# Performance work log

Hardware: AMD Instinct MI355X
Metric: run time of the kernel (lower is better)

## Reference

```python
import jax, jax.numpy as jnp
import numpy as np

B, N, D_IN, D_OUT = 4, 2048, 1024, 1024

def setup_inputs() -> dict:
    key = jax.random.key(0)
    ks = jax.random.split(key, 7)
    s_in = 1.0 / np.sqrt(D_IN)
    return {
        "X": jax.random.normal(ks[0], (B, N, D_IN), dtype=jnp.float32),
        "Wq": jax.random.uniform(ks[1], (D_IN, D_OUT), jnp.float32, -s_in, s_in),
        "bq": jax.random.uniform(ks[2], (D_OUT,), jnp.float32, -s_in, s_in),
        "Wk": jax.random.uniform(ks[3], (D_IN, D_OUT), jnp.float32, -s_in, s_in),
        "bk": jax.random.uniform(ks[4], (D_OUT,), jnp.float32, -s_in, s_in),
        "Wv": jax.random.uniform(ks[5], (D_IN, D_OUT), jnp.float32, -s_in, s_in),
        "bv": jax.random.uniform(ks[6], (D_OUT,), jnp.float32, -s_in, s_in),
    }

def reference(X, Wq, bq, Wk, bk, Wv, bv):
    # QKV projections: [B,N,D_in] @ [D_in,D_out] -> [B,N,D_out]
    q = jnp.einsum('bnd,de->bne', X, Wq) + bq
    k = jnp.einsum('bnd,de->bne', X, Wk) + bk
    v = jnp.einsum('bnd,de->bne', X, Wv) + bv
    # Unscaled attention (faithful: original has no 1/sqrt(d))
    scores = jnp.einsum('bne,bme->bnm', q, k)  # [B,N,N]
    weights = jax.nn.softmax(scores, axis=-1)
    return jnp.einsum('bnm,bme->bne', weights, v)
```

## Files before the change

### kernel.cpp

```cpp
#include <hip/hip_runtime.h>
#include <hip/hip_bf16.h>
#include <hip/hip_fp16.h>
#include <stdint.h>
#include <math.h>


typedef unsigned short ushort_t;
typedef __attribute__((ext_vector_type(8))) _Float16  f16x8;
typedef __attribute__((ext_vector_type(4))) _Float16  f16x4;
typedef __attribute__((ext_vector_type(4))) float     f32x4;

__device__ __forceinline__ void async_load16(const void* g, void* l) {
  __builtin_amdgcn_global_load_lds(
      (const __attribute__((address_space(1))) void*)g,
      (__attribute__((address_space(3))) void*)l, 16, 0, 0);
}

#define BARR do { __builtin_amdgcn_sched_barrier(0); \
                  __builtin_amdgcn_s_barrier();      \
                  __builtin_amdgcn_s_barrier();      \
                  __builtin_amdgcn_sched_barrier(0); } while (0)
#undef BARR
#define BARR do { __builtin_amdgcn_sched_barrier(0); \
                  __builtin_amdgcn_s_barrier();      \
                  __builtin_amdgcn_sched_barrier(0); } while (0)

#define A0OFF 0
#define B0OFF 16384
#define A1OFF 32768
#define B1OFF 49152

template<int SHIFT>
__device__ __forceinline__ void stage_half(const ushort_t* __restrict__ gb,
                                           int k0, int q, ushort_t* lt, int t)
{
#pragma unroll
  for (int j = 0; j < 2; ++j) {
    const int i   = j * 64 + (t >> 3);
    const int row = ((i >> SHIFT) << (SHIFT + 1)) | (q << SHIFT) | (i & ((1 << SHIFT) - 1));
    const int ch  = (t & 7) ^ (row & 7);
    async_load16(gb + (long)row * 1024 + k0 + ch * 8, lt + row * 64 + (t & 7) * 8);
  }
}

#define RD_A(TP, QM)                                                          \
  do { _Pragma("unroll") for (int m_ = 0; m_ < 4; ++m_) {                     \
    af[m_][0] = *(const f16x8*)&(TP)[(arow0 + (QM)*64 + m_*16) * 64 + ck0];   \
    af[m_][1] = *(const f16x8*)&(TP)[(arow0 + (QM)*64 + m_*16) * 64 + ck1];   \
  } } while (0)

#define RD_B(TP, QN)                                                          \
  do { _Pragma("unroll") for (int n_ = 0; n_ < 2; ++n_) {                     \
    bf[n_][0] = *(const f16x8*)&(TP)[(brow0 + (QN)*32 + n_*16) * 64 + ck0];   \
    bf[n_][1] = *(const f16x8*)&(TP)[(brow0 + (QN)*32 + n_*16) * 64 + ck1];   \
  } } while (0)

#define MM(QM, QN)                                                            \
  do { __builtin_amdgcn_s_setprio(1);                                         \
  _Pragma("unroll") for (int kh_ = 0; kh_ < 2; ++kh_)                         \
    _Pragma("unroll") for (int m_ = 0; m_ < 4; ++m_)                          \
      _Pragma("unroll") for (int n_ = 0; n_ < 2; ++n_)                        \
        acc[(QM)*4+m_][(QN)*2+n_] = __builtin_amdgcn_mfma_f32_16x16x32_f16(   \
            af[m_][kh_], bf[n_][kh_], acc[(QM)*4+m_][(QN)*2+n_], 0, 0, 0);    \
  __builtin_amdgcn_s_setprio(0); } while (0)

template<bool LAST>
__device__ __forceinline__ void iter256(const ushort_t* __restrict__ Ab,
                                        const ushort_t* __restrict__ Bb,
                                        ushort_t* lds, f32x4 (&acc)[8][4],
                                        int ka, int t, int arow0, int brow0,
                                        int ck0, int ck1)
{
  const int kb = ka + 64, kc = ka + 128, kd = ka + 192;
  f16x8 af[4][2], bf[2][2];

  RD_A(lds + A0OFF, 0); RD_B(lds + B0OFF, 0);
  stage_half<5>(Bb, kb, 0, lds + B1OFF, t);
  BARR; MM(0, 0); BARR;

  RD_B(lds + B0OFF, 1);
  if constexpr (!LAST) stage_half<6>(Ab, kc, 0, lds + A0OFF, t);
  BARR; MM(0, 1); BARR;

  RD_A(lds + A0OFF, 1);
  if constexpr (!LAST) stage_half<5>(Bb, kc, 1, lds + B0OFF, t);
  BARR; MM(1, 1); BARR;

  RD_B(lds + B0OFF, 0);
  if constexpr (!LAST) stage_half<6>(Ab, kc, 1, lds + A0OFF, t);
  BARR; MM(1, 0);
  if constexpr (LAST) asm volatile("s_waitcnt vmcnt(0)" ::: "memory");
  else                asm volatile("s_waitcnt vmcnt(6)" ::: "memory");
  BARR;

  RD_A(lds + A1OFF, 0); RD_B(lds + B1OFF, 0);
  if constexpr (!LAST) stage_half<5>(Bb, kc, 0, lds + B0OFF, t);
  BARR; MM(0, 0); BARR;

  RD_B(lds + B1OFF, 1);
  if constexpr (!LAST) stage_half<6>(Ab, kd, 0, lds + A1OFF, t);
  BARR; MM(0, 1); BARR;

  RD_A(lds + A1OFF, 1);
  if constexpr (!LAST) stage_half<5>(Bb, kd, 1, lds + B1OFF, t);
  BARR; MM(1, 1); BARR;

  RD_B(lds + B1OFF, 0);
  if constexpr (!LAST) stage_half<6>(Ab, kd, 1, lds + A1OFF, t);
  BARR; MM(1, 0);
  if constexpr (!LAST) asm volatile("s_waitcnt vmcnt(6)" ::: "memory");
  BARR;
}

__device__ __forceinline__ void gemm256(const ushort_t* __restrict__ Ab,
                                        const ushort_t* __restrict__ Bb,
                                        ushort_t* lds, f32x4 (&acc)[8][4])
{
  const int t    = threadIdx.x;
  const int lane = t & 63;
  const int wave = t >> 6;
  const int wr   = wave >> 2;
  const int wc   = wave & 3;
  const int arow0 = wr * 128 + (lane & 15);
  const int brow0 = wc * 64  + (lane & 15);
  const int ck0 = (((lane >> 4)    ) ^ (lane & 7)) * 8;
  const int ck1 = ((4 + (lane >> 4)) ^ (lane & 7)) * 8;

  stage_half<6>(Ab,  0, 0, lds + A0OFF, t);
  stage_half<5>(Bb,  0, 1, lds + B0OFF, t);
  stage_half<6>(Ab,  0, 1, lds + A0OFF, t);
  stage_half<5>(Bb,  0, 0, lds + B0OFF, t);
  stage_half<6>(Ab, 64, 0, lds + A1OFF, t);
  stage_half<5>(Bb, 64, 1, lds + B1OFF, t);
  stage_half<6>(Ab, 64, 1, lds + A1OFF, t);
  asm volatile("s_waitcnt vmcnt(6)" ::: "memory");
  BARR;

#pragma unroll 1
  for (int it = 0; it < 7; ++it)
    iter256<false>(Ab, Bb, lds, acc, it * 128, t, arow0, brow0, ck0, ck1);
  iter256<true>(Ab, Bb, lds, acc, 896, t, arow0, brow0, ck0, ck1);
}

#define NA0 0
#define NB0 16384
#define NA1 24576
#define NB1 40960

__device__ __forceinline__ void stage_h256(const ushort_t* __restrict__ gb, long ldk,
                                           int k0, int q, ushort_t* lt, int t)
{
#pragma unroll
  for (int j = 0; j < 2; ++j) {
    const int i   = j * 64 + (t >> 3);
    const int row = ((i >> 5) << 6) | (q << 5) | (i & 31);
    const int ch  = (t & 7) ^ (row & 7);
    async_load16(gb + (long)row * ldk + k0 + ch * 8, lt + row * 64 + (t & 7) * 8);
  }
}

__device__ __forceinline__ void stage_h128(const ushort_t* __restrict__ gb, long ldk,
                                           int k0, int q, ushort_t* lt, int t)
{
  const int i   = t >> 3;
  const int row = ((i >> 5) << 6) | (q << 5) | (i & 31);
  const int ch  = (t & 7) ^ (row & 7);
  async_load16(gb + (long)row * ldk + k0 + ch * 8, lt + row * 64 + (t & 7) * 8);
}

#define RD_A4(SET, BASE, QM)                                                  \
  do { _Pragma("unroll") for (int m_ = 0; m_ < 2; ++m_) {                     \
    SET[m_][0] = *(const f16x8*)&lds[(BASE) + (arow_l + (QM)*32 + m_*16) * 64 + ck0]; \
    SET[m_][1] = *(const f16x8*)&lds[(BASE) + (arow_l + (QM)*32 + m_*16) * 64 + ck1]; \
  } } while (0)

#define RD_B4(SET, BASE)                                                      \
  do { _Pragma("unroll") for (int q_ = 0; q_ < 2; ++q_)                       \
    _Pragma("unroll") for (int n_ = 0; n_ < 2; ++n_) {                        \
      SET[q_][n_][0] = *(const f16x8*)&lds[(BASE) + (brow_l + q_*32 + n_*16) * 64 + ck0]; \
      SET[q_][n_][1] = *(const f16x8*)&lds[(BASE) + (brow_l + q_*32 + n_*16) * 64 + ck1]; \
    } } while (0)

#define MM16(AS, BS, QM)                                                      \
  do { __builtin_amdgcn_s_setprio(1);                                         \
  _Pragma("unroll") for (int kh_ = 0; kh_ < 2; ++kh_)                         \
    _Pragma("unroll") for (int m_ = 0; m_ < 2; ++m_)                          \
      _Pragma("unroll") for (int n_ = 0; n_ < 2; ++n_) {                      \
        acc[(QM)*2+m_][n_]   = __builtin_amdgcn_mfma_f32_16x16x32_f16(        \
            AS[m_][kh_], BS[0][n_][kh_], acc[(QM)*2+m_][n_], 0, 0, 0);        \
        acc[(QM)*2+m_][2+n_] = __builtin_amdgcn_mfma_f32_16x16x32_f16(        \
            AS[m_][kh_], BS[1][n_][kh_], acc[(QM)*2+m_][2+n_], 0, 0, 0);      \
      }                                                                       \
  __builtin_amdgcn_s_setprio(0); } while (0)

#define MM16S(AS, BS, QM, SC)                                                 \
  do { __builtin_amdgcn_s_setprio(1);                                         \
  _Pragma("unroll") for (int m_ = 0; m_ < 2; ++m_)                            \
    _Pragma("unroll") for (int kh_ = 0; kh_ < 2; ++kh_) {                     \
      const f16x8 as_ = AS[m_][kh_] * (_Float16)(SC)[(QM)*2+m_];              \
      _Pragma("unroll") for (int n_ = 0; n_ < 2; ++n_) {                      \
        acc[(QM)*2+m_][n_]   = __builtin_amdgcn_mfma_f32_16x16x32_f16(        \
            as_, BS[0][n_][kh_], acc[(QM)*2+m_][n_], 0, 0, 0);                \
        acc[(QM)*2+m_][2+n_] = __builtin_amdgcn_mfma_f32_16x16x32_f16(        \
            as_, BS[1][n_][kh_], acc[(QM)*2+m_][2+n_], 0, 0, 0);              \
      } }                                                                     \
  __builtin_amdgcn_s_setprio(0); } while (0)

template<bool LAST>
__device__ __forceinline__ void iterRA(const ushort_t* __restrict__ Ab,
                                       const ushort_t* __restrict__ Bb,
                                       long lda, long ldb,
                                       ushort_t* lds, f32x4 (&acc)[4][4],
                                       int ka, int t, int arow_l, int brow_l,
                                       int ck0, int ck1,
                                       f16x8 (&aF)[2][2], f16x8 (&aG)[2][2],
                                       f16x8 (&bF)[2][2][2], f16x8 (&bG)[2][2][2])
{
  const int kc = ka + 128, kd = ka + 192;

  RD_A4(aG, NA0, 1);
  if constexpr (!LAST) { stage_h256(Ab, lda, kc, 0, lds + NA0, t);
                         stage_h128(Bb, ldb, kc, 0, lds + NB0, t); }
  BARR;
  MM16(aF, bF, 0);
  if constexpr (LAST) asm volatile("s_waitcnt vmcnt(0)" ::: "memory");
  else                asm volatile("s_waitcnt vmcnt(3)" ::: "memory");
  BARR;

  RD_A4(aF, NA1, 0);
  RD_B4(bG, NB1);
  if constexpr (!LAST) { stage_h256(Ab, lda, kc, 1, lds + NA0, t);
                         stage_h128(Bb, ldb, kc, 1, lds + NB0, t); }
  BARR;
  MM16(aG, bF, 1);
  BARR;

  RD_A4(aG, NA1, 1);
  if constexpr (!LAST) { stage_h256(Ab, lda, kd, 0, lds + NA1, t);
                         stage_h128(Bb, ldb, kd, 0, lds + NB1, t); }
  BARR;
  MM16(aF, bG, 0);
  if constexpr (!LAST) asm volatile("s_waitcnt vmcnt(3)" ::: "memory");
  BARR;

  if constexpr (!LAST) {
    RD_A4(aF, NA0, 0);
    RD_B4(bF, NB0);
    stage_h256(Ab, lda, kd, 1, lds + NA1, t);
    stage_h128(Bb, ldb, kd, 1, lds + NB1, t);
  }
  BARR;
  MM16(aG, bG, 1);
  BARR;
}

template<bool LAST>
__device__ __forceinline__ void pv_iterRA(const ushort_t* __restrict__ Ab,
                                          const ushort_t* __restrict__ Bb,
                                          ushort_t* lds, const float (*ScL)[256],
                                          f32x4 (&acc)[4][4],
                                          int ka, int t, int arow_l, int brow_l,
                                          int ck0, int ck1,
                                          f16x8 (&aF)[2][2], f16x8 (&aG)[2][2],
                                          f16x8 (&bF)[2][2][2], f16x8 (&bG)[2][2][2])
{
  const int kc = ka + 128, kd = ka + 192;
  const int cba = ka >> 6;
  float sa4[4], sb4[4];
#pragma unroll
  for (int s = 0; s < 4; ++s) {
    sa4[s] = ScL[cba][arow_l + s * 16];
    sb4[s] = ScL[cba + 1][arow_l + s * 16];
  }

  RD_A4(aG, NA0, 1);
  if constexpr (!LAST) { stage_h256(Ab, 2048, kc, 0, lds + NA0, t);
                         stage_h128(Bb, 2048, kc, 0, lds + NB0, t); }
  BARR;
  MM16S(aF, bF, 0, sa4);
  if constexpr (LAST) asm volatile("s_waitcnt vmcnt(0)" ::: "memory");
  else                asm volatile("s_waitcnt vmcnt(3)" ::: "memory");
  BARR;

  RD_A4(aF, NA1, 0);
  RD_B4(bG, NB1);
  if constexpr (!LAST) { stage_h256(Ab, 2048, kc, 1, lds + NA0, t);
                         stage_h128(Bb, 2048, kc, 1, lds + NB0, t); }
  BARR;
  MM16S(aG, bF, 1, sa4);
  BARR;

  RD_A4(aG, NA1, 1);
  if constexpr (!LAST) { stage_h256(Ab, 2048, kd, 0, lds + NA1, t);
                         stage_h128(Bb, 2048, kd, 0, lds + NB1, t); }
  BARR;
  MM16S(aF, bG, 0, sb4);
  if constexpr (!LAST) asm volatile("s_waitcnt vmcnt(3)" ::: "memory");
  BARR;

  if constexpr (!LAST) {
    RD_A4(aF, NA0, 0);
    RD_B4(bF, NB0);
    stage_h256(Ab, 2048, kd, 1, lds + NA1, t);
    stage_h128(Bb, 2048, kd, 1, lds + NB1, t);
  }
  BARR;
  MM16S(aG, bG, 1, sb4);
  BARR;
}

#define PROLOGUE_RA(LDA, LDB)                               \
  do {                                                      \
    stage_h256(Ab, (LDA),  0, 0, lds + NA0, t);             \
    stage_h128(Bb, (LDB),  0, 0, lds + NB0, t);             \
    stage_h256(Ab, (LDA),  0, 1, lds + NA0, t);             \
    stage_h128(Bb, (LDB),  0, 1, lds + NB0, t);             \
    asm volatile("s_waitcnt vmcnt(0)" ::: "memory");        \
    BARR;                                                   \
    RD_A4(aF, NA0, 0);                                      \
    RD_B4(bF, NB0);                                         \
    stage_h256(Ab, (LDA), 64, 0, lds + NA1, t);             \
    stage_h128(Bb, (LDB), 64, 0, lds + NB1, t);             \
    stage_h256(Ab, (LDA), 64, 1, lds + NA1, t);             \
    stage_h128(Bb, (LDB), 64, 1, lds + NB1, t);             \
    BARR;                                                   \
  } while (0)

__global__ __launch_bounds__(512, 2)
void qkproj_kernel(const ushort_t* __restrict__ A, const ushort_t* __restrict__ BT,
                   const float* __restrict__ bq, const float* __restrict__ bk,
                   __half* __restrict__ Qh, __half* __restrict__ Kh)
{
  __shared__ __align__(16) ushort_t lds[65536];

  const int nb = gridDim.x * gridDim.y;
  int id = blockIdx.y * gridDim.x + blockIdx.x;
  id = (id & 7) * (nb >> 3) + (id >> 3);
  const int bx = id % gridDim.x;
  const int by = id / gridDim.x;

  const ushort_t* Ab = A  + (long)by * 256 * 1024;
  const ushort_t* Bb = BT + (long)bx * 256 * 1024;

  f32x4 acc[8][4];
  const f32x4 zero = {0.0f, 0.0f, 0.0f, 0.0f};
#pragma unroll
  for (int i = 0; i < 8; ++i)
#pragma unroll
    for (int j = 0; j < 4; ++j) acc[i][j] = zero;

  gemm256(Ab, Bb, lds, acc);

  const int t = threadIdx.x, lane = t & 63, wave = t >> 6;
  const int wr = wave >> 2, wc = wave & 3;
  const int er = (lane >> 4) * 4, ec = lane & 15;
  const int tgt = bx >> 2;
  const float* bias = (tgt == 0) ? bq : bk;
  __half* o = (tgt == 0) ? Qh : Kh;

#pragma unroll
  for (int ni = 0; ni < 4; ++ni) {
    const int col = (bx & 3) * 256 + wc * 64 + ni * 16 + ec;
    const float bval = bias[col];
#pragma unroll
    for (int mi = 0; mi < 8; ++mi) {
      const long grow0 = (long)by * 256 + wr * 128 + mi * 16 + er;
#pragma unroll
      for (int r = 0; r < 4; ++r)
        o[(grow0 + r) * 1024 + col] = __float2half(acc[mi][ni][r] + bval);
    }
  }
}

__global__ __launch_bounds__(512, 2)
void vproj_kernel(const ushort_t* __restrict__ A, const ushort_t* __restrict__ BT,
                  const float* __restrict__ bvp, ushort_t* __restrict__ Vt)
{
  __shared__ __align__(16) ushort_t lds[49152];

  const int nb = gridDim.x * gridDim.y;
  int id = blockIdx.y * gridDim.x + blockIdx.x;
  id = (id & 7) * (nb >> 3) + (id >> 3);
  const int bx = id % gridDim.x;
  const int by = id / gridDim.x;

  const ushort_t* Ab = A  + (long)by * 256 * 1024;
  const ushort_t* Bb = BT + (long)(16 + bx) * 128 * 1024;

  const int t    = threadIdx.x;
  const int lane = t & 63;
  const int wave = t >> 6;
  const int wr   = wave >> 1;
  const int wc   = wave & 1;
  const int arow_l = wr * 64 + (lane & 15);
  const int brow_l = wc * 64 + (lane & 15);
  const int ck0 = (((lane >> 4)    ) ^ (lane & 7)) * 8;
  const int ck1 = ((4 + (lane >> 4)) ^ (lane & 7)) * 8;

  f32x4 acc[4][4];
  const f32x4 zero = {0.0f, 0.0f, 0.0f, 0.0f};
#pragma unroll
  for (int i = 0; i < 4; ++i)
#pragma unroll
    for (int j = 0; j < 4; ++j) acc[i][j] = zero;

  f16x8 aF[2][2], aG[2][2], bF[2][2][2], bG[2][2][2];

  PROLOGUE_RA(1024, 1024);
#pragma unroll 1
  for (int it = 0; it < 7; ++it)
    iterRA<false>(Ab, Bb, 1024, 1024, lds, acc, it * 128, t, arow_l, brow_l,
                  ck0, ck1, aF, aG, bF, bG);
  iterRA<true>(Ab, Bb, 1024, 1024, lds, acc, 896, t, arow_l, brow_l,
               ck0, ck1, aF, aG, bF, bG);

  const int er = (lane >> 4) * 4, ec = lane & 15;
#pragma unroll
  for (int ni = 0; ni < 4; ++ni) {
    const int col = bx * 128 + wc * 64 + ni * 16 + ec;
    const float bval = bvp[col];
#pragma unroll
    for (int mi = 0; mi < 4; ++mi) {
      const long grow0 = (long)by * 256 + wr * 64 + mi * 16 + er;
      const long b  = grow0 >> 11;
      const long ml = grow0 & 2047;
      f16x4 v4;
#pragma unroll
      for (int r = 0; r < 4; ++r) v4[r] = (_Float16)(acc[mi][ni][r] + bval);
      *(f16x4*)&Vt[b * 2097152 + (long)col * 2048 + ml] = v4;
    }
  }
}

__global__ __launch_bounds__(512, 2)
void qkattn_kernel(const ushort_t* __restrict__ Q, const ushort_t* __restrict__ Kh,
                   __half* __restrict__ S, float* __restrict__ PM, float* __restrict__ PS)
{
  __shared__ __align__(16) ushort_t lds[65536];

  const int nb = gridDim.x * gridDim.y;
  int id = blockIdx.y * gridDim.x + blockIdx.x;
  id = (id & 7) * (nb >> 3) + (id >> 3);
  const int bx = id % gridDim.x;
  const int by = id / gridDim.x;
  const long z = blockIdx.z;

  const ushort_t* Ab = Q  + z * 2048 * 1024 + (long)by * 256 * 1024;
  const ushort_t* Bb = Kh + z * 2048 * 1024 + (long)bx * 256 * 1024;
  __half* Sb = S + z * 2048 * 2048;

  f32x4 acc[8][4];
  const f32x4 zero = {0.0f, 0.0f, 0.0f, 0.0f};
#pragma unroll
  for (int i = 0; i < 8; ++i)
#pragma unroll
    for (int j = 0; j < 4; ++j) acc[i][j] = zero;

  gemm256(Ab, Bb, lds, acc);

  const int t = threadIdx.x, lane = t & 63, wave = t >> 6;
  const int wr = wave >> 2, wc = wave & 3;
  const int er = (lane >> 4) * 4, ec = lane & 15;
  const int cc = bx * 4 + wc;
  float* PMb = PM + z * 32 * 2048 + (long)cc * 2048;
  float* PSb = PS + z * 32 * 2048 + (long)cc * 2048;

#pragma unroll
  for (int m8 = 0; m8 < 8; ++m8)
#pragma unroll
    for (int r = 0; r < 4; ++r) {
      float m = fmaxf(fmaxf(acc[m8][0][r], acc[m8][1][r]),
                      fmaxf(acc[m8][2][r], acc[m8][3][r]));
      m = fmaxf(m, __shfl_xor(m, 1));
      m = fmaxf(m, __shfl_xor(m, 2));
      m = fmaxf(m, __shfl_xor(m, 4));
      m = fmaxf(m, __shfl_xor(m, 8));
      float s = 0.0f;
#pragma unroll
      for (int n4 = 0; n4 < 4; ++n4) {
        const float e = __expf(acc[m8][n4][r] - m);
        acc[m8][n4][r] = e;
        s += e;
      }
      s += __shfl_xor(s, 1);
      s += __shfl_xor(s, 2);
      s += __shfl_xor(s, 4);
      s += __shfl_xor(s, 8);
      if (ec == 0) {
        const long row = (long)by * 256 + wr * 128 + m8 * 16 + er + r;
        PMb[row] = m;
        PSb[row] = s;
      }
    }

#pragma unroll
  for (int n4 = 0; n4 < 4; ++n4) {
    const long col = (long)bx * 256 + wc * 64 + n4 * 16 + ec;
#pragma unroll
    for (int m8 = 0; m8 < 8; ++m8)
#pragma unroll
      for (int r = 0; r < 4; ++r) {
        const long grow = (long)by * 256 + wr * 128 + m8 * 16 + er + r;
        Sb[grow * 2048 + col] = __float2half(acc[m8][n4][r]);
      }
  }
}

__global__ __launch_bounds__(512, 2)
void pv_ra_kernel(const ushort_t* __restrict__ S, const ushort_t* __restrict__ Vt,
                  const float* __restrict__ PM, const float* __restrict__ PS,
                  float* __restrict__ Out)
{
  __shared__ __align__(16) ushort_t lds[49152];
  __shared__ float ScL[32][256];

  const int nb = gridDim.x * gridDim.y;
  int id = blockIdx.y * gridDim.x + blockIdx.x;
  id = (id & 7) * (nb >> 3) + (id >> 3);
  const int bx = id % gridDim.x;
  const int by = id / gridDim.x;
  const long z = blockIdx.z;

  const ushort_t* Ab = S  + z * 4194304 + (long)by * 256 * 2048;
  const ushort_t* Bb = Vt + z * 2097152 + (long)bx * 128 * 2048;
  float* Cb = Out + z * 2048 * 1024;

  const int t = threadIdx.x;

  if (t < 256) {
    const long row = (long)by * 256 + t;
    const float* PMb = PM + z * 32 * 2048;
    const float* PSb = PS + z * 32 * 2048;
    float pm[32];
    float m = -3.4e38f;
#pragma unroll
    for (int cb = 0; cb < 32; ++cb) {
      pm[cb] = PMb[(long)cb * 2048 + row];
      m = fmaxf(m, pm[cb]);
    }
    float l = 0.0f;
#pragma unroll
    for (int cb = 0; cb < 32; ++cb)
      l += PSb[(long)cb * 2048 + row] * __expf(pm[cb] - m);
    const float inv = 1.0f / l;
#pragma unroll
    for (int cb = 0; cb < 32; ++cb)
      ScL[cb][t] = __expf(pm[cb] - m) * inv;
  }
  __syncthreads();

  const int lane = t & 63;
  const int wave = t >> 6;
  const int wr   = wave >> 1;
  const int wc   = wave & 1;
  const int arow_l = wr * 64 + (lane & 15);
  const int brow_l = wc * 64 + (lane & 15);
  const int ck0 = (((lane >> 4)    ) ^ (lane & 7)) * 8;
  const int ck1 = ((4 + (lane >> 4)) ^ (lane & 7)) * 8;

  f32x4 acc[4][4];
  const f32x4 zero = {0.0f, 0.0f, 0.0f, 0.0f};
#pragma unroll
  for (int i = 0; i < 4; ++i)
#pragma unroll
    for (int j = 0; j < 4; ++j) acc[i][j] = zero;

  f16x8 aF[2][2], aG[2][2], bF[2][2][2], bG[2][2][2];

  PROLOGUE_RA(2048, 2048);
#pragma unroll 1
  for (int it = 0; it < 15; ++it)
    pv_iterRA<false>(Ab, Bb, lds, ScL, acc, it * 128, t, arow_l, brow_l,
                     ck0, ck1, aF, aG, bF, bG);
  pv_iterRA<true>(Ab, Bb, lds, ScL, acc, 1920, t, arow_l, brow_l,
                  ck0, ck1, aF, aG, bF, bG);

  const int er = (lane >> 4) * 4, ec = lane & 15;
#pragma unroll
  for (int ni = 0; ni < 4; ++ni) {
    const int gcol = bx * 128 + wc * 64 + ni * 16 + ec;
#pragma unroll
    for (int mi = 0; mi < 4; ++mi) {
#pragma unroll
      for (int r = 0; r < 4; ++r) {
        const long grow = (long)by * 256 + wr * 64 + mi * 16 + er + r;
        Cb[grow * 1024 + gcol] = acc[mi][ni][r];
      }
    }
  }
}

__global__ __launch_bounds__(256)
void prep_kernel(const float* __restrict__ W0, const float* __restrict__ W1,
                 const float* __restrict__ W2, __half* __restrict__ dstW,
                 const float* __restrict__ X, __half* __restrict__ Xh)
{
  __shared__ float tile[32][33];
  const int z = blockIdx.z;
  if (z < 3) {
    const float* src = (z == 0) ? W0 : (z == 1) ? W1 : W2;
    __half* d = dstW + (long)z * 1024 * 1024;
    const int c0 = blockIdx.x * 32;
    const int r0 = blockIdx.y * 32;
    const int tx = threadIdx.x & 31;
    const int ty = threadIdx.x >> 5;
#pragma unroll
    for (int i = 0; i < 32; i += 8)
      tile[ty + i][tx] = src[(long)(r0 + ty + i) * 1024 + (c0 + tx)];
    __syncthreads();
#pragma unroll
    for (int i = 0; i < 32; i += 8)
      d[(long)(c0 + ty + i) * 1024 + (r0 + tx)] = __float2half(tile[tx][ty + i]);
  } else {
    const int bid = blockIdx.y * gridDim.x + blockIdx.x;
    const long i = (((long)(z - 3) * 1024 + bid) * 256 + threadIdx.x) * 8;
    const float4 a = *(const float4*)(X + i);
    const float4 b = *(const float4*)(X + i + 4);
    f16x8 h;
    h[0] = (_Float16)a.x; h[1] = (_Float16)a.y; h[2] = (_Float16)a.z; h[3] = (_Float16)a.w;
    h[4] = (_Float16)b.x; h[5] = (_Float16)b.y; h[6] = (_Float16)b.z; h[7] = (_Float16)b.w;
    *(f16x8*)((ushort_t*)Xh + i) = h;
  }
}

extern "C" void kernel_launch(void* const* d_in, const int* in_sizes, int n_in,
                              void* d_out, int out_size, void* d_ws, size_t ws_size,
                              hipStream_t stream)
{
  const int  Bb = 4, Nn = 2048, Dd = 1024;
  const long BN = (long)Bb * Nn;

  const float* X  = (const float*)d_in[0];
  const float* Wq = (const float*)d_in[1];
  const float* bq = (const float*)d_in[2];
  const float* Wk = (const float*)d_in[3];
  const float* bk = (const float*)d_in[4];
  const float* Wv = (const float*)d_in[5];
  const float* bv = (const float*)d_in[6];
  float* Out      = (float*)d_out;

  uint8_t* w = (uint8_t*)d_ws;
  ushort_t* Wt = (ushort_t*)w;  w += (size_t)3 * Dd * Dd * 2;

  const size_t statsBytes = (size_t)Bb * 32 * Nn * 4;
  const size_t fullNeed = (size_t)3 * Dd * Dd * 2
                        + 4 * ((size_t)BN * Dd * 2)
                        + (size_t)Bb * Nn * Nn * 2
                        + 2 * statsBytes;

  if (ws_size >= fullNeed) {
    ushort_t* Xh = (ushort_t*)w;  w += (size_t)BN * Dd * 2;
    ushort_t* Q  = (ushort_t*)w;  w += (size_t)BN * Dd * 2;
    ushort_t* Kb = (ushort_t*)w;  w += (size_t)BN * Dd * 2;
    ushort_t* Vt = (ushort_t*)w;  w += (size_t)BN * Dd * 2;
    ushort_t* S  = (ushort_t*)w;  w += (size_t)Bb * Nn * Nn * 2;
    float*    PM = (float*)w;     w += statsBytes;
    float*    PS = (float*)w;

    prep_kernel<<<dim3(32, 32, 7), 256, 0, stream>>>(Wq, Wk, Wv, (__half*)Wt, X, (__half*)Xh);

    qkproj_kernel<<<dim3(8, BN / 256, 1), 512, 0, stream>>>(
        Xh, Wt, bq, bk, (__half*)Q, (__half*)Kb);

    vproj_kernel<<<dim3(8, BN / 256, 1), 512, 0, stream>>>(Xh, Wt, bv, Vt);

    qkattn_kernel<<<dim3(Nn / 256, Nn / 256, Bb), 512, 0, stream>>>(
        Q, Kb, (__half*)S, PM, PS);

    pv_ra_kernel<<<dim3(Dd / 128, Nn / 256, Bb), 512, 0, stream>>>(
        S, Vt, PM, PS, Out);
  } else {
    ushort_t* Xh = (ushort_t*)w;  w += (size_t)Nn * Dd * 2;
    ushort_t* Q  = (ushort_t*)w;  w += (size_t)Nn * Dd * 2;
    ushort_t* Kb = (ushort_t*)w;  w += (size_t)Nn * Dd * 2;
    ushort_t* Vt = (ushort_t*)w;  w += (size_t)Nn * Dd * 2;
    ushort_t* S  = (ushort_t*)w;  w += (size_t)Nn * Nn * 2;
    float*    PM = (float*)w;     w += (size_t)32 * Nn * 4;
    float*    PS = (float*)w;

    for (int b = 0; b < Bb; ++b) {
      const float* Xb = X + (long)b * Nn * Dd;
      prep_kernel<<<dim3(32, 32, b == 0 ? 4 : 1), 256, 0, stream>>>(
          Wq, Wk, Wv, (__half*)Wt, Xb, (__half*)Xh);
      qkproj_kernel<<<dim3(8, Nn / 256, 1), 512, 0, stream>>>(
          Xh, Wt, bq, bk, (__half*)Q, (__half*)Kb);
      vproj_kernel<<<dim3(8, Nn / 256, 1), 512, 0, stream>>>(Xh, Wt, bv, Vt);
      qkattn_kernel<<<dim3(Nn / 256, Nn / 256, 1), 512, 0, stream>>>(
          Q, Kb, (__half*)S, PM, PS);
      pv_ra_kernel<<<dim3(Dd / 128, Nn / 256, 1), 512, 0, stream>>>(
          S, Vt, PM, PS, Out + (long)b * Nn * Dd);
    }
  }
}
```

Measured before the change: 258.7 us.

## Stage GEMM epilogues through LDS for coalesced 16-byte global stores

The qkproj, vproj and qkattn epilogues now write fp16 results into a per-wave LDS tile, then read them back as 8-element vectors so each global store is a coalesced 16-byte write instead of scattered 2-byte stores. The qkattn softmax row statistics are batched so that all max and sum shuffle reductions run over 32 rows at once, which gives more instruction-level parallelism. The vproj launch is moved ahead of qkproj, and a duplicated BARR definition is cleaned up. The LDS staging adds extra LDS traffic and waitcnt stalls, and it relies on the mainloop LDS buffers being free when the epilogue reuses them.

```diff
diff --git a/kernel.cpp b/kernel.cpp
--- a/kernel.cpp
+++ b/kernel.cpp
@@ -18,12 +18,10 @@
 
 #define BARR do { __builtin_amdgcn_sched_barrier(0); \
                   __builtin_amdgcn_s_barrier();      \
-                  __builtin_amdgcn_s_barrier();      \
                   __builtin_amdgcn_sched_barrier(0); } while (0)
-#undef BARR
-#define BARR do { __builtin_amdgcn_sched_barrier(0); \
-                  __builtin_amdgcn_s_barrier();      \
-                  __builtin_amdgcn_sched_barrier(0); } while (0)
+
+#define LGKM0 do { asm volatile("s_waitcnt lgkmcnt(0)" ::: "memory"); \
+                   __builtin_amdgcn_sched_barrier(0); } while (0)
 
 #define A0OFF 0
 #define B0OFF 16384
@@ -353,21 +351,38 @@
 
   const int t = threadIdx.x, lane = t & 63, wave = t >> 6;
   const int wr = wave >> 2, wc = wave & 3;
-  const int er = (lane >> 4) * 4, ec = lane & 15;
+  const int er4 = (lane >> 4) * 4, ec = lane & 15;
   const int tgt = bx >> 2;
   const float* bias = (tgt == 0) ? bq : bk;
   __half* o = (tgt == 0) ? Qh : Kh;
 
-#pragma unroll
-  for (int ni = 0; ni < 4; ++ni) {
-    const int col = (bx & 3) * 256 + wc * 64 + ni * 16 + ec;
-    const float bval = bias[col];
-#pragma unroll
-    for (int mi = 0; mi < 8; ++mi) {
-      const long grow0 = (long)by * 256 + wr * 128 + mi * 16 + er;
-#pragma unroll
-      for (int r = 0; r < 4; ++r)
-        o[(grow0 + r) * 1024 + col] = __float2half(acc[mi][ni][r] + bval);
+  float bv[4];
+#pragma unroll
+  for (int n4 = 0; n4 < 4; ++n4)
+    bv[n4] = bias[(bx & 3) * 256 + wc * 64 + n4 * 16 + ec];
+
+  _Float16* ws = (_Float16*)lds + wave * 4608;
+  const long gr0 = (long)by * 256 + wr * 128;
+  const int  gc0 = (bx & 3) * 256 + wc * 64;
+
+#pragma unroll
+  for (int h = 0; h < 2; ++h) {
+    LGKM0;
+#pragma unroll
+    for (int m4 = 0; m4 < 4; ++m4)
+#pragma unroll
+      for (int n4 = 0; n4 < 4; ++n4)
+#pragma unroll
+        for (int r = 0; r < 4; ++r)
+          ws[(m4 * 16 + er4 + r) * 72 + n4 * 16 + ec] =
+              (_Float16)(acc[h * 4 + m4][n4][r] + bv[n4]);
+    LGKM0;
+#pragma unroll
+    for (int p = 0; p < 8; ++p) {
+      const int lrow = p * 8 + (lane >> 3);
+      const int coff = (lane & 7) * 8;
+      const f16x8 v = *(const f16x8*)&ws[lrow * 72 + coff];
+      *(f16x8*)((_Float16*)o + (gr0 + h * 64 + lrow) * 1024 + gc0 + coff) = v;
     }
   }
 }
@@ -414,21 +429,30 @@
   iterRA<true>(Ab, Bb, 1024, 1024, lds, acc, 896, t, arow_l, brow_l,
                ck0, ck1, aF, aG, bF, bG);
 
-  const int er = (lane >> 4) * 4, ec = lane & 15;
+  const int er4 = (lane >> 4) * 4, ec = lane & 15;
+
+  _Float16* ws = (_Float16*)lds + wave * 4608;
+  LGKM0;
 #pragma unroll
   for (int ni = 0; ni < 4; ++ni) {
-    const int col = bx * 128 + wc * 64 + ni * 16 + ec;
-    const float bval = bvp[col];
+    const float bval = bvp[bx * 128 + wc * 64 + ni * 16 + ec];
 #pragma unroll
     for (int mi = 0; mi < 4; ++mi) {
-      const long grow0 = (long)by * 256 + wr * 64 + mi * 16 + er;
-      const long b  = grow0 >> 11;
-      const long ml = grow0 & 2047;
       f16x4 v4;
 #pragma unroll
       for (int r = 0; r < 4; ++r) v4[r] = (_Float16)(acc[mi][ni][r] + bval);
-      *(f16x4*)&Vt[b * 2097152 + (long)col * 2048 + ml] = v4;
+      *(f16x4*)&ws[(ni * 16 + ec) * 72 + mi * 16 + er4] = v4;
     }
+  }
+  LGKM0;
+  const long b   = by >> 3;
+  const int  mlb = ((by * 256) & 2047) + wr * 64;
+#pragma unroll
+  for (int p = 0; p < 8; ++p) {
+    const int lcol = p * 8 + (lane >> 3);
+    const int moff = (lane & 7) * 8;
+    const f16x8 v = *(const f16x8*)&ws[lcol * 72 + moff];
+    *(f16x8*)&Vt[b * 2097152 + (long)(bx * 128 + wc * 64 + lcol) * 2048 + mlb + moff] = v;
   }
 }
 
@@ -460,49 +484,73 @@
 
   const int t = threadIdx.x, lane = t & 63, wave = t >> 6;
   const int wr = wave >> 2, wc = wave & 3;
-  const int er = (lane >> 4) * 4, ec = lane & 15;
+  const int er4 = (lane >> 4) * 4, ec = lane & 15;
   const int cc = bx * 4 + wc;
   float* PMb = PM + z * 32 * 2048 + (long)cc * 2048;
   float* PSb = PS + z * 32 * 2048 + (long)cc * 2048;
 
+  float mrow[32], srow[32];
 #pragma unroll
   for (int m8 = 0; m8 < 8; ++m8)
 #pragma unroll
+    for (int r = 0; r < 4; ++r)
+      mrow[m8 * 4 + r] = fmaxf(fmaxf(acc[m8][0][r], acc[m8][1][r]),
+                               fmaxf(acc[m8][2][r], acc[m8][3][r]));
+#pragma unroll
+  for (int st = 1; st <= 8; st <<= 1)
+#pragma unroll
+    for (int i = 0; i < 32; ++i)
+      mrow[i] = fmaxf(mrow[i], __shfl_xor(mrow[i], st));
+#pragma unroll
+  for (int m8 = 0; m8 < 8; ++m8)
+#pragma unroll
     for (int r = 0; r < 4; ++r) {
-      float m = fmaxf(fmaxf(acc[m8][0][r], acc[m8][1][r]),
-                      fmaxf(acc[m8][2][r], acc[m8][3][r]));
-      m = fmaxf(m, __shfl_xor(m, 1));
-      m = fmaxf(m, __shfl_xor(m, 2));
-      m = fmaxf(m, __shfl_xor(m, 4));
-      m = fmaxf(m, __shfl_xor(m, 8));
       float s = 0.0f;
 #pragma unroll
       for (int n4 = 0; n4 < 4; ++n4) {
-        const float e = __expf(acc[m8][n4][r] - m);
+        const float e = __expf(acc[m8][n4][r] - mrow[m8 * 4 + r]);
         acc[m8][n4][r] = e;
         s += e;
       }
-      s += __shfl_xor(s, 1);
-      s += __shfl_xor(s, 2);
-      s += __shfl_xor(s, 4);
-      s += __shfl_xor(s, 8);
-      if (ec == 0) {
-        const long row = (long)by * 256 + wr * 128 + m8 * 16 + er + r;
-        PMb[row] = m;
-        PSb[row] = s;
-      }
+      srow[m8 * 4 + r] = s;
     }
-
-#pragma unroll
-  for (int n4 = 0; n4 < 4; ++n4) {
-    const long col = (long)bx * 256 + wc * 64 + n4 * 16 + ec;
-#pragma unroll
-    for (int m8 = 0; m8 < 8; ++m8)
-#pragma unroll
-      for (int r = 0; r < 4; ++r) {
-        const long grow = (long)by * 256 + wr * 128 + m8 * 16 + er + r;
-        Sb[grow * 2048 + col] = __float2half(acc[m8][n4][r]);
-      }
+#pragma unroll
+  for (int st = 1; st <= 8; st <<= 1)
+#pragma unroll
+    for (int i = 0; i < 32; ++i)
+      srow[i] += __shfl_xor(srow[i], st);
+
+  if (ec == 0) {
+#pragma unroll
+    for (int i = 0; i < 32; ++i) {
+      const long row = (long)by * 256 + wr * 128 + (i >> 2) * 16 + er4 + (i & 3);
+      PMb[row] = mrow[i];
+      PSb[row] = srow[i];
+    }
+  }
+
+  _Float16* ws = (_Float16*)lds + wave * 4608;
+  const long gr0 = (long)by * 256 + wr * 128;
+  const int  gc0 = bx * 256 + wc * 64;
+#pragma unroll
+  for (int h = 0; h < 2; ++h) {
+    LGKM0;
+#pragma unroll
+    for (int m4 = 0; m4 < 4; ++m4)
+#pragma unroll
+      for (int n4 = 0; n4 < 4; ++n4)
+#pragma unroll
+        for (int r = 0; r < 4; ++r)
+          ws[(m4 * 16 + er4 + r) * 72 + n4 * 16 + ec] =
+              (_Float16)acc[h * 4 + m4][n4][r];
+    LGKM0;
+#pragma unroll
+    for (int p = 0; p < 8; ++p) {
+      const int lrow = p * 8 + (lane >> 3);
+      const int coff = (lane & 7) * 8;
+      const f16x8 v = *(const f16x8*)&ws[lrow * 72 + coff];
+      *(f16x8*)((_Float16*)Sb + (gr0 + h * 64 + lrow) * 2048 + gc0 + coff) = v;
+    }
   }
 }
 
@@ -575,7 +623,7 @@
   pv_iterRA<true>(Ab, Bb, lds, ScL, acc, 1920, t, arow_l, brow_l,
                   ck0, ck1, aF, aG, bF, bG);
 
-  const int er = (lane >> 4) * 4, ec = lane & 15;
+  const int er4 = (lane >> 4) * 4, ec = lane & 15;
 #pragma unroll
   for (int ni = 0; ni < 4; ++ni) {
     const int gcol = bx * 128 + wc * 64 + ni * 16 + ec;
@@ -583,7 +631,7 @@
     for (int mi = 0; mi < 4; ++mi) {
 #pragma unroll
       for (int r = 0; r < 4; ++r) {
-        const long grow = (long)by * 256 + wr * 64 + mi * 16 + er + r;
+        const long grow = (long)by * 256 + wr * 64 + mi * 16 + er4 + r;
         Cb[grow * 1024 + gcol] = acc[mi][ni][r];
       }
     }
@@ -659,10 +707,10 @@
 
     prep_kernel<<<dim3(32, 32, 7), 256, 0, stream>>>(Wq, Wk, Wv, (__half*)Wt, X, (__half*)Xh);
 
+    vproj_kernel<<<dim3(8, BN / 256, 1), 512, 0, stream>>>(Xh, Wt, bv, Vt);
+
     qkproj_kernel<<<dim3(8, BN / 256, 1), 512, 0, stream>>>(
         Xh, Wt, bq, bk, (__half*)Q, (__half*)Kb);
-
-    vproj_kernel<<<dim3(8, BN / 256, 1), 512, 0, stream>>>(Xh, Wt, bv, Vt);
 
     qkattn_kernel<<<dim3(Nn / 256, Nn / 256, Bb), 512, 0, stream>>>(
         Q, Kb, (__half*)S, PM, PS);
@@ -682,9 +730,9 @@
       const float* Xb = X + (long)b * Nn * Dd;
       prep_kernel<<<dim3(32, 32, b == 0 ? 4 : 1), 256, 0, stream>>>(
           Wq, Wk, Wv, (__half*)Wt, Xb, (__half*)Xh);
+      vproj_kernel<<<dim3(8, Nn / 256, 1), 512, 0, stream>>>(Xh, Wt, bv, Vt);
       qkproj_kernel<<<dim3(8, Nn / 256, 1), 512, 0, stream>>>(
           Xh, Wt, bq, bk, (__half*)Q, (__half*)Kb);
-      vproj_kernel<<<dim3(8, Nn / 256, 1), 512, 0, stream>>>(Xh, Wt, bv, Vt);
       qkattn_kernel<<<dim3(Nn / 256, Nn / 256, 1), 512, 0, stream>>>(
           Q, Kb, (__half*)S, PM, PS);
       pv_ra_kernel<<<dim3(Dd / 128, Nn / 256, 1), 512, 0, stream>>>(
```

Result: faster. 246.0 us (-4.9%).
